# Kernel optimization log

Hardware: AMD Instinct MI355X
Metric: run time of the kernel (lower is better)

The kernel has to match this reference:

```python
import jax, jax.numpy as jnp
import numpy as np

N_EMBD = 1024
N_HEADS = 16
HEAD_DIM = N_EMBD // N_HEADS


def setup_inputs() -> dict:
    key = jax.random.key(0)
    ks = jax.random.split(key, 6)
    s = 1.0 / np.sqrt(N_EMBD)
    x = jax.random.normal(ks[0], (2, 2048, N_EMBD), dtype=jnp.float32)
    # torch Linear weights are [out, in]; y = x @ W.T
    Wk = jax.random.uniform(ks[1], (N_EMBD, N_EMBD), jnp.float32, -s, s)
    Wq = jax.random.uniform(ks[2], (N_EMBD, N_EMBD), jnp.float32, -s, s)
    Wv = jax.random.uniform(ks[3], (N_EMBD, N_EMBD), jnp.float32, -s, s)
    Wp = jax.random.uniform(ks[4], (N_EMBD, N_EMBD), jnp.float32, -s, s)
    bp = jax.random.uniform(ks[5], (N_EMBD,), jnp.float32, -s, s)
    return {"x": x, "Wq": Wq, "Wk": Wk, "Wv": Wv, "Wp": Wp, "bp": bp}


def reference(x, Wq, Wk, Wv, Wp, bp):
    B, T, C = x.shape
    H, D = N_HEADS, HEAD_DIM
    # projections (torch Linear: x @ W.T), reshape to [B, H, T, D]
    q = (x @ Wq.T).reshape(B, T, H, D).transpose(0, 2, 1, 3)
    k = (x @ Wk.T).reshape(B, T, H, D).transpose(0, 2, 1, 3)
    v = (x @ Wv.T).reshape(B, T, H, D).transpose(0, 2, 1, 3)
    # scaled causal attention, full [B,H,T,T] scores (faithful to original)
    att = jnp.einsum('bhqd,bhkd->bhqk', q, k) * (D ** -0.5)
    causal = jnp.tril(jnp.ones((T, T), dtype=bool))
    att = jnp.where(causal[None, None], att, -jnp.inf)
    att = jax.nn.softmax(att, axis=-1)
    out = jnp.einsum('bhqk,bhkd->bhqd', att, v)
    out = out.transpose(0, 2, 1, 3).reshape(B, T, C)
    return out @ Wp.T + bp
```

## Files before the change

### kernel.cpp

```cpp
#include <hip/hip_runtime.h>

typedef __bf16 bf16;
typedef __bf16 bf16x8 __attribute__((ext_vector_type(8)));
typedef float f32x4 __attribute__((ext_vector_type(4)));

typedef __attribute__((address_space(1))) const void as1_void;
typedef __attribute__((address_space(3))) void as3_void;

#define DEV __device__ __forceinline__
#define NEG_BIG (-1.0e30f)


DEV void async_load16(const void* g, void* l) {
  __builtin_amdgcn_global_load_lds((as1_void*)g, (as3_void*)l, 16, 0, 0);
}
DEV bf16x8 load8(const bf16* p) { bf16x8 v; __builtin_memcpy(&v, p, 16); return v; }
DEV void store8(bf16* p, bf16x8 v) { __builtin_memcpy(p, &v, 16); }

DEV int sniff_bf16(const unsigned short* __restrict__ xr) {
  const int lane = threadIdx.x & 63;
  const unsigned short w = xr[lane * 2];
  const int e = (w >> 7) & 0xFF;
  const bool sane = ((w & 0x7FFF) == 0) || (e >= 97 && e <= 157);
  return __popcll(__ballot(sane)) >= 48;
}

struct ConvArgs {
  const void* src[6];
  bf16* dst[6];
  int n[6];
};

__global__ __launch_bounds__(256) void convert_kernel(ConvArgs a) {
  const int isbf = sniff_bf16((const unsigned short*)a.src[0]);
  const int t = blockIdx.y;
  const int n = a.n[t];
  bf16* d = a.dst[t];
  const int stride = gridDim.x * 256 * 8;
  if (isbf) {
    const bf16* s = (const bf16*)a.src[t];
    for (int i = (blockIdx.x * 256 + threadIdx.x) * 8; i < n; i += stride)
      store8(d + i, load8(s + i));
  } else {
    const float* s = (const float*)a.src[t];
    for (int i = (blockIdx.x * 256 + threadIdx.x) * 8; i < n; i += stride) {
      float tmp[8];
      __builtin_memcpy(tmp, s + i, 32);
      bf16x8 v;
#pragma unroll
      for (int j = 0; j < 8; ++j) v[j] = (bf16)tmp[j];
      store8(d + i, v);
    }
  }
}

DEV void gemm_core_128(const bf16* A, const bf16* W, int K, int m0, int n0,
                       f32x4 (&acc)[4][4]) {
  __shared__ alignas(16) bf16 As[128 * 64];
  __shared__ alignas(16) bf16 Bs[128 * 64];
  const int tid = threadIdx.x;
  const int lane = tid & 63;
  const int wid = tid >> 6;
  const int wm = (wid >> 1) << 6;
  const int wn = (wid & 1) << 6;
  const int lr = lane & 15;
  const int lg = lane >> 4;

  const f32x4 zero = {0.f, 0.f, 0.f, 0.f};
#pragma unroll
  for (int i = 0; i < 4; ++i)
#pragma unroll
    for (int j = 0; j < 4; ++j) acc[i][j] = zero;

  for (int k0 = 0; k0 < K; k0 += 64) {
#pragma unroll
    for (int it = 0; it < 4; ++it) {
      const int lin = it * 256 + tid;
      const int row = lin >> 3;
      const int sc = (lin & 7) ^ (row & 7);
      async_load16(A + (size_t)(m0 + row) * K + (size_t)(k0 + sc * 8), As + lin * 8);
      async_load16(W + (size_t)(n0 + row) * K + (size_t)(k0 + sc * 8), Bs + lin * 8);
    }
    __syncthreads();
#pragma unroll
    for (int kk = 0; kk < 64; kk += 32) {
      const int g0 = kk >> 3;
      bf16x8 af[4], bfr[4];
#pragma unroll
      for (int i = 0; i < 4; ++i) {
        const int r = wm + i * 16 + lr;
        af[i] = load8(As + ((r << 3) | ((g0 + lg) ^ (r & 7))) * 8);
      }
#pragma unroll
      for (int j = 0; j < 4; ++j) {
        const int r = wn + j * 16 + lr;
        bfr[j] = load8(Bs + ((r << 3) | ((g0 + lg) ^ (r & 7))) * 8);
      }
#pragma unroll
      for (int i = 0; i < 4; ++i)
#pragma unroll
        for (int j = 0; j < 4; ++j)
          acc[i][j] = __builtin_amdgcn_mfma_f32_16x16x32_bf16(af[i], bfr[j], acc[i][j], 0, 0, 0);
    }
    __syncthreads();
  }
}

DEV size_t frag_idx(int row, int col) {
  return ((size_t)(((col >> 5) * 4 + ((row >> 4) & 3)) * 64 + ((col >> 3) & 3) * 16 + (row & 15)) << 3)
         | (size_t)(col & 7);
}

__global__ __launch_bounds__(256) void qkv_proj_kernel(
    const bf16* __restrict__ x, const bf16* __restrict__ Wq,
    const bf16* __restrict__ Wk, const bf16* __restrict__ Wv,
    bf16* __restrict__ q_ws, bf16* __restrict__ k_ws, bf16* __restrict__ vt_ws) {
  const int L = blockIdx.x;
  const int xcd = L & 7;
  const int i2 = L >> 3;
  const int m0 = (xcd * 4 + (i2 & 3)) << 7;
  const int rest = i2 >> 2;
  const int n0 = (rest & 7) << 7;
  const int mode = rest >> 3;
  const bf16* W = (mode == 0) ? Wq : (mode == 1) ? Wk : Wv;
  f32x4 acc[4][4];
  gemm_core_128(x, W, 1024, m0, n0, acc);

  const int tid = threadIdx.x;
  const int lane = tid & 63, wid = tid >> 6;
  const int wm = (wid >> 1) << 6, wn = (wid & 1) << 6;
  const int lr = lane & 15, lg = lane >> 4;
  bf16* out = (mode == 0) ? q_ws : (mode == 1) ? k_ws : vt_ws;
#pragma unroll
  for (int i = 0; i < 4; ++i) {
#pragma unroll
    for (int r = 0; r < 4; ++r) {
      const int m = m0 + wm + i * 16 + lg * 4 + r;
      const int b = m >> 11, t = m & 2047;
#pragma unroll
      for (int j = 0; j < 4; ++j) {
        const int n = n0 + wn + j * 16 + lr;
        const int h = n >> 6, d = n & 63;
        const float v = acc[i][j][r];
        const size_t base = ((size_t)(b * 16 + h) << 17) + ((size_t)(t >> 6) << 12);
        const size_t idx = base + ((mode < 2) ? frag_idx(t & 63, d) : frag_idx(d, t & 63));
        out[idx] = (bf16)v;
      }
    }
  }
}

__global__ __launch_bounds__(256, 2) void attn_kernel(
    const bf16* __restrict__ q_ws, const bf16* __restrict__ k_ws,
    const bf16* __restrict__ vt_ws, bf16* __restrict__ a_ws) {
  const int L = blockIdx.x;
  const int xcd = L & 7;
  const int bh = xcd * 4 + ((L >> 3) & 3);
  const int pr = L >> 5;
  const int tid = threadIdx.x;
  const int lane = tid & 63, w = tid >> 6;
  const int lr = lane & 15, lg = lane >> 4;
  const int fo = lg * 16 + lr;

  __shared__ alignas(16) bf16 Ps[4][16 * 72];
  bf16* ps = &Ps[w][0];

  const size_t hb = (size_t)bh << 17;
  const int b = bh >> 4, h = bh & 15;
  const f32x4 zero = {0.f, 0.f, 0.f, 0.f};

  for (int ph = 0; ph < 2; ++ph) {
    const int qt = ph ? (31 - pr) : pr;
    const size_t qtb = hb + ((size_t)qt << 12);

    bf16x8 aq[2];
#pragma unroll
    for (int c2 = 0; c2 < 2; ++c2)
      aq[c2] = load8(q_ws + qtb + (size_t)(((c2 * 4 + w) * 64 + fo) << 3));

    f32x4 o_acc[4];
#pragma unroll
    for (int j = 0; j < 4; ++j) o_acc[j] = zero;
    float lsum[4] = {0.f, 0.f, 0.f, 0.f};

    auto load_k = [&](bf16x8 (&bk)[4][2], int kt) {
      const size_t ktb = hb + ((size_t)kt << 12);
#pragma unroll
      for (int j = 0; j < 4; ++j)
#pragma unroll
        for (int c2 = 0; c2 < 2; ++c2)
          bk[j][c2] = load8(k_ws + ktb + (size_t)(((c2 * 4 + j) * 64 + fo) << 3));
    };

    auto step = [&](const bf16x8 (&bk)[4][2], int kt, bool diag) {
      const size_t ktb = hb + ((size_t)kt << 12);
      bf16x8 bv[4][2];
#pragma unroll
      for (int j = 0; j < 4; ++j)
#pragma unroll
        for (int c2 = 0; c2 < 2; ++c2)
          bv[j][c2] = load8(vt_ws + ktb + (size_t)(((c2 * 4 + j) * 64 + fo) << 3));

      f32x4 s[4];
#pragma unroll
      for (int j = 0; j < 4; ++j) {
        s[j] = __builtin_amdgcn_mfma_f32_16x16x32_bf16(aq[0], bk[j][0], zero, 0, 0, 0);
        s[j] = __builtin_amdgcn_mfma_f32_16x16x32_bf16(aq[1], bk[j][1], s[j], 0, 0, 0);
      }
      float p[4][4];
#pragma unroll
      for (int j = 0; j < 4; ++j) {
#pragma unroll
        for (int r = 0; r < 4; ++r) {
          float v = s[j][r] * 0.125f;
          if (diag && (j * 16 + lr) > (w * 16 + lg * 4 + r)) v = NEG_BIG;
          p[j][r] = __expf(v);
        }
      }
#pragma unroll
      for (int r = 0; r < 4; ++r)
        lsum[r] += (p[0][r] + p[1][r]) + (p[2][r] + p[3][r]);
#pragma unroll
      for (int j = 0; j < 4; ++j)
#pragma unroll
        for (int r = 0; r < 4; ++r)
          ps[(lg * 4 + r) * 72 + j * 16 + lr] = (bf16)p[j][r];
#pragma unroll
      for (int c2 = 0; c2 < 2; ++c2) {
        const bf16x8 ap = load8(ps + lr * 72 + c2 * 32 + lg * 8);
#pragma unroll
        for (int j = 0; j < 4; ++j)
          o_acc[j] = __builtin_amdgcn_mfma_f32_16x16x32_bf16(ap, bv[j][c2], o_acc[j], 0, 0, 0);
      }
    };

    bf16x8 bkA[4][2], bkB[4][2];
    const int n = qt;
    load_k(bkA, qt);
    if (n > 0) load_k(bkB, 0);
    step(bkA, qt, true);
    int kt = 0;
    while (kt + 1 < n) {
      load_k(bkA, kt + 1);
      step(bkB, kt, false);
      if (kt + 2 < n) load_k(bkB, kt + 2);
      step(bkA, kt + 1, false);
      kt += 2;
    }
    if (kt < n) step(bkB, kt, false);

    float l_i[4];
#pragma unroll
    for (int r = 0; r < 4; ++r) {
      float v = lsum[r];
#pragma unroll
      for (int off = 1; off < 16; off <<= 1) v += __shfl_xor(v, off, 64);
      l_i[r] = v;
    }

#pragma unroll
    for (int r = 0; r < 4; ++r) {
      const int t = qt * 64 + w * 16 + lg * 4 + r;
      const float inv = 1.f / l_i[r];
#pragma unroll
      for (int j = 0; j < 4; ++j) {
        const size_t idx = (((size_t)(b * 2048 + t)) << 10) | (size_t)(h * 64 + j * 16 + lr);
        a_ws[idx] = (bf16)(o_acc[j][r] * inv);
      }
    }
  }
}

__global__ __launch_bounds__(256) void out_proj_kernel(
    const bf16* __restrict__ A, const bf16* __restrict__ Wp,
    const bf16* __restrict__ bp, void* __restrict__ out,
    const unsigned short* __restrict__ xraw) {
  const int L = blockIdx.x;
  const int xcd = L & 7;
  const int i2 = L >> 3;
  const int m0 = (xcd * 4 + (i2 & 3)) << 7;
  const int n0 = (i2 >> 2) << 7;
  f32x4 acc[4][4];
  gemm_core_128(A, Wp, 1024, m0, n0, acc);

  const int tid = threadIdx.x;
  const int lane = tid & 63, wid = tid >> 6;
  const int wm = (wid >> 1) << 6, wn = (wid & 1) << 6;
  const int lr = lane & 15, lg = lane >> 4;
  const int isbf = sniff_bf16(xraw);
#pragma unroll
  for (int i = 0; i < 4; ++i) {
#pragma unroll
    for (int r = 0; r < 4; ++r) {
      const int m = m0 + wm + i * 16 + lg * 4 + r;
#pragma unroll
      for (int j = 0; j < 4; ++j) {
        const int n = n0 + wn + j * 16 + lr;
        const float v = acc[i][j][r] + (float)bp[n];
        const size_t idx = ((size_t)m << 10) | (size_t)n;
        if (isbf) ((bf16*)out)[idx] = (bf16)v;
        else      ((float*)out)[idx] = v;
      }
    }
  }
}

extern "C" void kernel_launch(void* const* d_in, const int* in_sizes, int n_in,
                              void* d_out, int out_size, void* d_ws, size_t ws_size,
                              hipStream_t stream) {
  (void)in_sizes; (void)n_in; (void)out_size;
  if (ws_size < (50u << 20)) return;

  char* ws = (char*)d_ws;
  bf16* q_ws  = (bf16*)(ws);
  bf16* k_ws  = (bf16*)(ws + (8u << 20));
  bf16* vt_ws = (bf16*)(ws + (16u << 20));
  bf16* a_ws  = (bf16*)(ws + (24u << 20));
  bf16* xc    = (bf16*)(ws + (32u << 20));
  bf16* Wqc   = (bf16*)(ws + (40u << 20));
  bf16* Wkc   = (bf16*)(ws + (42u << 20));
  bf16* Wvc   = (bf16*)(ws + (44u << 20));
  bf16* Wpc   = (bf16*)(ws + (46u << 20));
  bf16* bpc   = (bf16*)(ws + (48u << 20));

  ConvArgs ca;
  ca.src[0] = d_in[0]; ca.dst[0] = xc;  ca.n[0] = 4096 * 1024;
  ca.src[1] = d_in[1]; ca.dst[1] = Wqc; ca.n[1] = 1024 * 1024;
  ca.src[2] = d_in[2]; ca.dst[2] = Wkc; ca.n[2] = 1024 * 1024;
  ca.src[3] = d_in[3]; ca.dst[3] = Wvc; ca.n[3] = 1024 * 1024;
  ca.src[4] = d_in[4]; ca.dst[4] = Wpc; ca.n[4] = 1024 * 1024;
  ca.src[5] = d_in[5]; ca.dst[5] = bpc; ca.n[5] = 1024;
  convert_kernel<<<dim3(512, 6), 256, 0, stream>>>(ca);

  qkv_proj_kernel<<<768, 256, 0, stream>>>(xc, Wqc, Wkc, Wvc, q_ws, k_ws, vt_ws);
  attn_kernel<<<512, 256, 0, stream>>>(q_ws, k_ws, vt_ws, a_ws);
  out_proj_kernel<<<256, 256, 0, stream>>>(a_ws, Wpc, bpc, d_out,
                                           (const unsigned short*)d_in[0]);
}
```

Measured before the change: 190.5 us.

## Double-buffer LDS tiles in GEMM core to overlap async loads with MFMA

Adds a second LDS buffer for the A and W tiles in the shared 128x128 GEMM core. The next tile's async global-to-LDS loads now run while the current tile is being computed, with explicit vmcnt waits and barriers replacing the per-iteration syncthreads. The goal is to hide global load latency behind MFMA work. In exchange LDS use doubles to 64KB per block, which may reduce occupancy, and correctness depends on the hand-written vmcnt counts matching the 8 loads issued per stage.

```diff
diff --git a/kernel.cpp b/kernel.cpp
--- a/kernel.cpp
+++ b/kernel.cpp
@@ -56,8 +56,8 @@
 
 DEV void gemm_core_128(const bf16* A, const bf16* W, int K, int m0, int n0,
                        f32x4 (&acc)[4][4]) {
-  __shared__ alignas(16) bf16 As[128 * 64];
-  __shared__ alignas(16) bf16 Bs[128 * 64];
+  __shared__ alignas(16) bf16 As[2][128 * 64];
+  __shared__ alignas(16) bf16 Bs[2][128 * 64];
   const int tid = threadIdx.x;
   const int lane = tid & 63;
   const int wid = tid >> 6;
@@ -72,16 +72,25 @@
 #pragma unroll
     for (int j = 0; j < 4; ++j) acc[i][j] = zero;
 
-  for (int k0 = 0; k0 < K; k0 += 64) {
+  const int nt = K >> 6;
+
+  auto stage = [&](int buf, int t) {
+    const int k0 = t << 6;
 #pragma unroll
     for (int it = 0; it < 4; ++it) {
       const int lin = it * 256 + tid;
       const int row = lin >> 3;
       const int sc = (lin & 7) ^ (row & 7);
-      async_load16(A + (size_t)(m0 + row) * K + (size_t)(k0 + sc * 8), As + lin * 8);
-      async_load16(W + (size_t)(n0 + row) * K + (size_t)(k0 + sc * 8), Bs + lin * 8);
-    }
-    __syncthreads();
+      async_load16(A + (size_t)(m0 + row) * K + (size_t)(k0 + sc * 8),
+                   &As[buf][0] + lin * 8);
+      async_load16(W + (size_t)(n0 + row) * K + (size_t)(k0 + sc * 8),
+                   &Bs[buf][0] + lin * 8);
+    }
+  };
+
+  auto compute = [&](int buf) {
+    const bf16* as = &As[buf][0];
+    const bf16* bs = &Bs[buf][0];
 #pragma unroll
     for (int kk = 0; kk < 64; kk += 32) {
       const int g0 = kk >> 3;
@@ -89,12 +98,12 @@
 #pragma unroll
       for (int i = 0; i < 4; ++i) {
         const int r = wm + i * 16 + lr;
-        af[i] = load8(As + ((r << 3) | ((g0 + lg) ^ (r & 7))) * 8);
+        af[i] = load8(as + ((r << 3) | ((g0 + lg) ^ (r & 7))) * 8);
       }
 #pragma unroll
       for (int j = 0; j < 4; ++j) {
         const int r = wn + j * 16 + lr;
-        bfr[j] = load8(Bs + ((r << 3) | ((g0 + lg) ^ (r & 7))) * 8);
+        bfr[j] = load8(bs + ((r << 3) | ((g0 + lg) ^ (r & 7))) * 8);
       }
 #pragma unroll
       for (int i = 0; i < 4; ++i)
@@ -102,7 +111,20 @@
         for (int j = 0; j < 4; ++j)
           acc[i][j] = __builtin_amdgcn_mfma_f32_16x16x32_bf16(af[i], bfr[j], acc[i][j], 0, 0, 0);
     }
-    __syncthreads();
+  };
+
+  stage(0, 0);
+  stage(1, 1);
+  int cur = 0;
+  for (int t = 0; t < nt; ++t) {
+    if (t + 1 < nt) asm volatile("s_waitcnt vmcnt(8)" ::: "memory");
+    else            asm volatile("s_waitcnt vmcnt(0)" ::: "memory");
+    __builtin_amdgcn_s_barrier();
+    compute(cur);
+    asm volatile("s_waitcnt lgkmcnt(0)" ::: "memory");
+    __builtin_amdgcn_s_barrier();
+    if (t + 2 < nt) stage(cur, t + 2);
+    cur ^= 1;
   }
 }
 
```

Measured after the change: 182.2 us. 4.4% less time.

## Replace LDS-tiled 128x128 GEMM with single-wave 64x64 register-fed GEMM

Applied to the files above, without the earlier changes.

The projection GEMMs stop staging tiles in shared memory. Each 64-thread block now computes a 64x64 output tile, loading MFMA fragments straight from global memory into registers with a two-stage double buffer. This removes the LDS traffic and the block barriers, and launches four times as many small blocks. In exchange, operands are no longer shared across waves, so global and L2 traffic per FLOP rises, and the 16-byte per-lane row loads are poorly coalesced.

```diff
diff --git a/kernel.cpp b/kernel.cpp
--- a/kernel.cpp
+++ b/kernel.cpp
@@ -4,16 +4,10 @@
 typedef __bf16 bf16x8 __attribute__((ext_vector_type(8)));
 typedef float f32x4 __attribute__((ext_vector_type(4)));
 
-typedef __attribute__((address_space(1))) const void as1_void;
-typedef __attribute__((address_space(3))) void as3_void;
-
 #define DEV __device__ __forceinline__
 #define NEG_BIG (-1.0e30f)
 
 
-DEV void async_load16(const void* g, void* l) {
-  __builtin_amdgcn_global_load_lds((as1_void*)g, (as3_void*)l, 16, 0, 0);
-}
 DEV bf16x8 load8(const bf16* p) { bf16x8 v; __builtin_memcpy(&v, p, 16); return v; }
 DEV void store8(bf16* p, bf16x8 v) { __builtin_memcpy(p, &v, 16); }
 
@@ -54,17 +48,17 @@
   }
 }
 
-DEV void gemm_core_128(const bf16* A, const bf16* W, int K, int m0, int n0,
-                       f32x4 (&acc)[4][4]) {
-  __shared__ alignas(16) bf16 As[128 * 64];
-  __shared__ alignas(16) bf16 Bs[128 * 64];
-  const int tid = threadIdx.x;
-  const int lane = tid & 63;
-  const int wid = tid >> 6;
-  const int wm = (wid >> 1) << 6;
-  const int wn = (wid & 1) << 6;
-  const int lr = lane & 15;
-  const int lg = lane >> 4;
+DEV void gemm_wave64(const bf16* __restrict__ A, const bf16* __restrict__ W,
+                     const int K, int m0, int n0, f32x4 (&acc)[4][4]) {
+  const int lane = threadIdx.x & 63;
+  const int lr = lane & 15, lg = lane >> 4;
+
+  const bf16* pa[4];
+  const bf16* pb[4];
+#pragma unroll
+  for (int i = 0; i < 4; ++i) pa[i] = A + (size_t)(m0 + i * 16 + lr) * K + lg * 8;
+#pragma unroll
+  for (int j = 0; j < 4; ++j) pb[j] = W + (size_t)(n0 + j * 16 + lr) * K + lg * 8;
 
   const f32x4 zero = {0.f, 0.f, 0.f, 0.f};
 #pragma unroll
@@ -72,37 +66,33 @@
 #pragma unroll
     for (int j = 0; j < 4; ++j) acc[i][j] = zero;
 
-  for (int k0 = 0; k0 < K; k0 += 64) {
-#pragma unroll
-    for (int it = 0; it < 4; ++it) {
-      const int lin = it * 256 + tid;
-      const int row = lin >> 3;
-      const int sc = (lin & 7) ^ (row & 7);
-      async_load16(A + (size_t)(m0 + row) * K + (size_t)(k0 + sc * 8), As + lin * 8);
-      async_load16(W + (size_t)(n0 + row) * K + (size_t)(k0 + sc * 8), Bs + lin * 8);
-    }
-    __syncthreads();
-#pragma unroll
-    for (int kk = 0; kk < 64; kk += 32) {
-      const int g0 = kk >> 3;
-      bf16x8 af[4], bfr[4];
-#pragma unroll
-      for (int i = 0; i < 4; ++i) {
-        const int r = wm + i * 16 + lr;
-        af[i] = load8(As + ((r << 3) | ((g0 + lg) ^ (r & 7))) * 8);
-      }
-#pragma unroll
-      for (int j = 0; j < 4; ++j) {
-        const int r = wn + j * 16 + lr;
-        bfr[j] = load8(Bs + ((r << 3) | ((g0 + lg) ^ (r & 7))) * 8);
-      }
-#pragma unroll
-      for (int i = 0; i < 4; ++i)
-#pragma unroll
-        for (int j = 0; j < 4; ++j)
-          acc[i][j] = __builtin_amdgcn_mfma_f32_16x16x32_bf16(af[i], bfr[j], acc[i][j], 0, 0, 0);
-    }
-    __syncthreads();
+  bf16x8 aA[4], bA[4], aB[4], bB[4];
+
+  auto loadset = [&](int h, bf16x8 (&af)[4], bf16x8 (&bf)[4]) {
+#pragma unroll
+    for (int i = 0; i < 4; ++i) af[i] = load8(pa[i] + h * 32);
+#pragma unroll
+    for (int j = 0; j < 4; ++j) bf[j] = load8(pb[j] + h * 32);
+  };
+  auto mm = [&](const bf16x8 (&af)[4], const bf16x8 (&bf)[4]) {
+#pragma unroll
+    for (int i = 0; i < 4; ++i)
+#pragma unroll
+      for (int j = 0; j < 4; ++j)
+        acc[i][j] = __builtin_amdgcn_mfma_f32_16x16x32_bf16(af[i], bf[j], acc[i][j], 0, 0, 0);
+  };
+
+  loadset(0, aA, bA);
+  loadset(1, aB, bB);
+#pragma unroll
+  for (int h = 0; h < 32; ++h) {
+    if ((h & 1) == 0) {
+      mm(aA, bA);
+      if (h + 2 < 32) loadset(h + 2, aA, bA);
+    } else {
+      mm(aB, bB);
+      if (h + 2 < 32) loadset(h + 2, aB, bB);
+    }
   }
 }
 
@@ -111,35 +101,33 @@
          | (size_t)(col & 7);
 }
 
-__global__ __launch_bounds__(256) void qkv_proj_kernel(
+__global__ __launch_bounds__(64) void qkv_proj_kernel(
     const bf16* __restrict__ x, const bf16* __restrict__ Wq,
     const bf16* __restrict__ Wk, const bf16* __restrict__ Wv,
     bf16* __restrict__ q_ws, bf16* __restrict__ k_ws, bf16* __restrict__ vt_ws) {
   const int L = blockIdx.x;
   const int xcd = L & 7;
   const int i2 = L >> 3;
-  const int m0 = (xcd * 4 + (i2 & 3)) << 7;
-  const int rest = i2 >> 2;
-  const int n0 = (rest & 7) << 7;
-  const int mode = rest >> 3;
+  const int m0 = (xcd * 8 + (i2 & 7)) << 6;
+  const int rest = i2 >> 3;
+  const int n0 = (rest & 15) << 6;
+  const int mode = rest >> 4;
   const bf16* W = (mode == 0) ? Wq : (mode == 1) ? Wk : Wv;
   f32x4 acc[4][4];
-  gemm_core_128(x, W, 1024, m0, n0, acc);
-
-  const int tid = threadIdx.x;
-  const int lane = tid & 63, wid = tid >> 6;
-  const int wm = (wid >> 1) << 6, wn = (wid & 1) << 6;
+  gemm_wave64(x, W, 1024, m0, n0, acc);
+
+  const int lane = threadIdx.x & 63;
   const int lr = lane & 15, lg = lane >> 4;
   bf16* out = (mode == 0) ? q_ws : (mode == 1) ? k_ws : vt_ws;
 #pragma unroll
   for (int i = 0; i < 4; ++i) {
 #pragma unroll
     for (int r = 0; r < 4; ++r) {
-      const int m = m0 + wm + i * 16 + lg * 4 + r;
+      const int m = m0 + i * 16 + lg * 4 + r;
       const int b = m >> 11, t = m & 2047;
 #pragma unroll
       for (int j = 0; j < 4; ++j) {
-        const int n = n0 + wn + j * 16 + lr;
+        const int n = n0 + j * 16 + lr;
         const int h = n >> 6, d = n & 63;
         const float v = acc[i][j][r];
         const size_t base = ((size_t)(b * 16 + h) << 17) + ((size_t)(t >> 6) << 12);
@@ -271,31 +259,29 @@
   }
 }
 
-__global__ __launch_bounds__(256) void out_proj_kernel(
+__global__ __launch_bounds__(64) void out_proj_kernel(
     const bf16* __restrict__ A, const bf16* __restrict__ Wp,
     const bf16* __restrict__ bp, void* __restrict__ out,
     const unsigned short* __restrict__ xraw) {
   const int L = blockIdx.x;
   const int xcd = L & 7;
   const int i2 = L >> 3;
-  const int m0 = (xcd * 4 + (i2 & 3)) << 7;
-  const int n0 = (i2 >> 2) << 7;
+  const int m0 = (xcd * 8 + (i2 & 7)) << 6;
+  const int n0 = (i2 >> 3) << 6;
   f32x4 acc[4][4];
-  gemm_core_128(A, Wp, 1024, m0, n0, acc);
-
-  const int tid = threadIdx.x;
-  const int lane = tid & 63, wid = tid >> 6;
-  const int wm = (wid >> 1) << 6, wn = (wid & 1) << 6;
+  gemm_wave64(A, Wp, 1024, m0, n0, acc);
+
+  const int lane = threadIdx.x & 63;
   const int lr = lane & 15, lg = lane >> 4;
   const int isbf = sniff_bf16(xraw);
 #pragma unroll
   for (int i = 0; i < 4; ++i) {
 #pragma unroll
     for (int r = 0; r < 4; ++r) {
-      const int m = m0 + wm + i * 16 + lg * 4 + r;
-#pragma unroll
-      for (int j = 0; j < 4; ++j) {
-        const int n = n0 + wn + j * 16 + lr;
+      const int m = m0 + i * 16 + lg * 4 + r;
+#pragma unroll
+      for (int j = 0; j < 4; ++j) {
+        const int n = n0 + j * 16 + lr;
         const float v = acc[i][j][r] + (float)bp[n];
         const size_t idx = ((size_t)m << 10) | (size_t)n;
         if (isbf) ((bf16*)out)[idx] = (bf16)v;
@@ -332,8 +318,8 @@
   ca.src[5] = d_in[5]; ca.dst[5] = bpc; ca.n[5] = 1024;
   convert_kernel<<<dim3(512, 6), 256, 0, stream>>>(ca);
 
-  qkv_proj_kernel<<<768, 256, 0, stream>>>(xc, Wqc, Wkc, Wvc, q_ws, k_ws, vt_ws);
+  qkv_proj_kernel<<<3072, 64, 0, stream>>>(xc, Wqc, Wkc, Wvc, q_ws, k_ws, vt_ws);
   attn_kernel<<<512, 256, 0, stream>>>(q_ws, k_ws, vt_ws, a_ws);
-  out_proj_kernel<<<256, 256, 0, stream>>>(a_ws, Wpc, bpc, d_out,
+  out_proj_kernel<<<1024, 64, 0, stream>>>(a_ws, Wpc, bpc, d_out,
                                            (const unsigned short*)d_in[0]);
 }
```

New measurement: 266.4 us. 1.4x slower.
